# Optimization experiments

Measured on AMD Instinct MI355X. Metric: run time of the kernel, lower is better.

## Reference

```python
import jax, jax.numpy as jnp
import numpy as np


def gcn_conv(x, W, b, src, dst, num_nodes):
    # PyG GCNConv: h = D^{-1/2} (A + I) D^{-1/2} (x W) + b
    h = x @ W  # [N, H]
    ones = jnp.ones(src.shape[0], dtype=h.dtype)
    deg = jax.ops.segment_sum(ones, dst, num_segments=num_nodes) + 1.0  # +1 for self-loop
    d_inv_sqrt = jax.lax.rsqrt(deg)
    norm = d_inv_sqrt[src] * d_inv_sqrt[dst]  # [E]
    msg = h[src] * norm[:, None]  # [E, H] gather
    agg = jax.ops.segment_sum(msg, dst, num_segments=num_nodes)  # scatter-add
    agg = agg + h * (1.0 / deg)[:, None]  # self-loop term: deg_i^{-1/2} * deg_i^{-1/2}
    return agg + b


def setup_inputs() -> dict:
    key = jax.random.key(0)
    ks = jax.random.split(key, 10)
    N, E, F, H, C, G = 100000, 1000000, 64, 128, 2, 512
    x = jax.random.normal(ks[0], (N, F), dtype=jnp.float32)
    edge_index = jax.random.randint(ks[1], (2, E), 0, N, dtype=jnp.int64)
    batch = jnp.sort(jax.random.randint(ks[2], (N,), 0, G, dtype=jnp.int64))
    s1 = 1.0 / np.sqrt(F)
    s2 = 1.0 / np.sqrt(H)
    W1 = jax.random.normal(ks[3], (F, H), dtype=jnp.float32) * s1
    b1 = jnp.zeros((H,), dtype=jnp.float32)
    W2 = jax.random.normal(ks[4], (H, H), dtype=jnp.float32) * s2
    b2 = jnp.zeros((H,), dtype=jnp.float32)
    Wfc = jax.random.normal(ks[5], (H, C), dtype=jnp.float32) * s2
    bfc = jnp.zeros((C,), dtype=jnp.float32)
    return {"x": x, "edge_index": edge_index, "batch": batch, "num_graphs": G,
            "W1": W1, "b1": b1, "W2": W2, "b2": b2, "Wfc": Wfc, "bfc": bfc}


def reference(x, edge_index, batch, num_graphs, W1, b1, W2, b2, Wfc, bfc):
    # Dropout is inference-mode (identity), matching model.eval().
    N = x.shape[0]
    src, dst = edge_index[0], edge_index[1]
    h = gcn_conv(x, W1, b1, src, dst, N)
    h = jax.nn.relu(h)
    h = gcn_conv(h, W2, b2, src, dst, N)
    h = jax.nn.relu(h)
    # global mean pool over graphs
    summed = jax.ops.segment_sum(h, batch, num_segments=num_graphs)  # [G, H]
    counts = jax.ops.segment_sum(jnp.ones((N,), h.dtype), batch, num_segments=num_graphs)
    pooled = summed / jnp.maximum(counts, 1.0)[:, None]
    logits = pooled @ Wfc + bfc  # [G, C]
    return jax.nn.softmax(logits, axis=1)
```

## Files before the change

### kernel.cpp

```cpp
#include <hip/hip_runtime.h>
#include <hip/hip_bf16.h>

typedef __hip_bfloat16 bf16;
typedef __attribute__((ext_vector_type(8))) short short8;
typedef __attribute__((ext_vector_type(4))) float f32x4;
typedef __attribute__((ext_vector_type(2))) float f32x2;

#define FDIM 64
#define HDIM 128

#define ESTRIDE 4096
#define EC 8192
#define ECPT (EC / 256)

__device__ __forceinline__ float b2f(bf16 v) { return __bfloat162float(v); }
__device__ __forceinline__ float bits2f(unsigned int u) {
    return __uint_as_float(u << 16);
}
__device__ __forceinline__ unsigned short f2bits(float f) {
    bf16 b = __float2bfloat16(f);
    return *reinterpret_cast<unsigned short*>(&b);
}
__device__ __forceinline__ unsigned char f2fp8(float v) {
    int pk = __builtin_amdgcn_cvt_pk_fp8_f32(v, v, 0, false);
    return (unsigned char)(pk & 0xFF);
}

__global__ __launch_bounds__(256) void k_prep_flags(const unsigned short* __restrict__ w1u,
                                                    const int* __restrict__ edge,
                                                    const int* __restrict__ batch,
                                                    int* __restrict__ flags,
                                                    int* __restrict__ zbase, int zn4) {
    if (blockIdx.x == 0 && threadIdx.x < 192) {
        int wave = threadIdx.x >> 6, lane = threadIdx.x & 63;
        if (wave == 0) {
            int wild = 0;
#pragma unroll
            for (int r = 0; r < 2; r++) {
                int i = 2 * lane + 128 * r;
                int e = (w1u[i] >> 7) & 0xFF;
                wild += (e == 0 || e >= 137) ? 1 : 0;
            }
            for (int s = 32; s; s >>= 1) wild += __shfl_down(wild, s);
            if (lane == 0) flags[0] = (wild > 16) ? 1 : 0;
        } else if (wave == 1) {
            int z = 0;
#pragma unroll
            for (int r = 0; r < 2; r++) {
                int i = 2 * lane + 1 + 128 * r;
                z += (edge[i] == 0) ? 1 : 0;
            }
            for (int s = 32; s; s >>= 1) z += __shfl_down(z, s);
            if (lane == 0) flags[1] = (z > 64) ? 1 : 0;
        } else {
            int z = 0;
#pragma unroll
            for (int r = 0; r < 2; r++) {
                int i = 1025 + 2 * lane + 128 * r;
                z += (batch[i] == 0) ? 1 : 0;
            }
            for (int s = 32; s; s >>= 1) z += __shfl_down(z, s);
            if (lane == 0) flags[2] = (z > 64) ? 1 : 0;
        }
    }
    int4 zz = make_int4(0, 0, 0, 0);
    int stride = gridDim.x * 256;
    for (int t = blockIdx.x * 256 + threadIdx.x; t < zn4; t += stride)
        ((int4*)zbase)[t] = zz;
}

__device__ __forceinline__ int edge_word(const int* e, long long logical_idx, int is64) {
    return is64 ? e[2 * logical_idx] : e[logical_idx];
}

__global__ __launch_bounds__(256) void k_phase1(const int* __restrict__ edge,
                                                int* __restrict__ gcur,
                                                int* __restrict__ ebuf,
                                                int E,
                                                const void* __restrict__ W1, const void* __restrict__ b1,
                                                const void* __restrict__ W2, const void* __restrict__ b2,
                                                const void* __restrict__ Wfc, const void* __restrict__ bfc,
                                                bf16* __restrict__ W1t, bf16* __restrict__ W2t,
                                                bf16* __restrict__ b1c, bf16* __restrict__ b2c,
                                                bf16* __restrict__ Wfcc, bf16* __restrict__ bfcc,
                                                const void* __restrict__ x,
                                                unsigned char* __restrict__ X8,
                                                int totalX4, const int* __restrict__ flags,
                                                const int* __restrict__ batch,
                                                int* __restrict__ gstart,
                                                int N, int G,
                                                int NB1, int WB, int XB) {
    int blk = blockIdx.x;
    if (blk < NB1) {
        __shared__ int h[512];
        int tid = threadIdx.x;
        for (int b2 = tid; b2 < 512; b2 += 256) h[b2] = 0;
        __syncthreads();
        int is64 = flags[1];
        int e0 = blk * EC;
        int dcache[ECPT];
#pragma unroll
        for (int k = 0; k < ECPT; k++) {
            int i = e0 + (k << 8) + tid;
            int d = -1;
            if (i < E) d = edge_word(edge, (long long)E + i, is64);
            dcache[k] = d;
            if (d >= 0) atomicAdd(&h[(d >> 8) & 511], 1);
        }
        __syncthreads();
        for (int b2 = tid; b2 < 512; b2 += 256) {
            int c = h[b2];
            h[b2] = c ? atomicAdd(&gcur[b2], c) : 0;
        }
        __syncthreads();
#pragma unroll
        for (int k = 0; k < ECPT; k++) {
            int i = e0 + (k << 8) + tid;
            int d = dcache[k];
            if (d >= 0) {
                int s = edge_word(edge, i, is64);
                int bb = (d >> 8) & 511;
                int pos = atomicAdd(&h[bb], 1);
                if ((unsigned)pos < (unsigned)ESTRIDE)
                    ebuf[(bb << 12) + pos] = s | ((d & 255) << 24);
            }
        }
    } else if (blk < NB1 + WB) {
        int f0 = flags[0];
        int gid = (blk - NB1) * 256 + threadIdx.x;
        int stride = WB * 256;
#define CV(src, si) (f0 ? __float2bfloat16(((const float*)(src))[si]) : ((const bf16*)(src))[si])
        for (int i = gid; i < FDIM * HDIM; i += stride) {
            int n = i >> 6, k = i & 63;
            W1t[i] = CV(W1, k * HDIM + n);
        }
        for (int i = gid; i < HDIM * HDIM; i += stride) {
            int n = i >> 7, k = i & 127;
            W2t[i] = CV(W2, k * HDIM + n);
        }
        for (int i = gid; i < HDIM; i += stride) b1c[i] = CV(b1, i);
        for (int i = gid; i < HDIM; i += stride) b2c[i] = CV(b2, i);
        for (int i = gid; i < HDIM * 2; i += stride) Wfcc[i] = CV(Wfc, i);
        for (int i = gid; i < 2; i += stride) bfcc[i] = CV(bfc, i);
#undef CV
    } else if (blk < NB1 + WB + XB) {
        int t = (blk - NB1 - WB) * 256 + threadIdx.x;
        if (t >= totalX4) return;
        float4 v;
        if (flags[0]) {
            v = ((const float4*)x)[t];
        } else {
            uint2 p = ((const uint2*)x)[t];
            v.x = bits2f(p.x & 0xFFFFu); v.y = bits2f(p.x >> 16);
            v.z = bits2f(p.y & 0xFFFFu); v.w = bits2f(p.y >> 16);
        }
        unsigned int q0 = (unsigned int)__builtin_amdgcn_cvt_pk_fp8_f32(v.x, v.y, 0, false) & 0xFFFFu;
        unsigned int q1 = (unsigned int)__builtin_amdgcn_cvt_pk_fp8_f32(v.z, v.w, 0, false) & 0xFFFFu;
        ((unsigned int*)X8)[t] = (q1 << 16) | q0;
    } else {
        int i = (blk - NB1 - WB - XB) * 256 + threadIdx.x;
        if (i >= N) return;
        int is64 = flags[2];
        int bi = is64 ? batch[2 * i] : batch[i];
        if (i == 0) {
            for (int g = 0; g <= bi; g++) gstart[g] = 0;
        } else {
            int bp = is64 ? batch[2 * (i - 1)] : batch[i - 1];
            for (int g = bp + 1; g <= bi; g++) gstart[g] = i;
        }
        if (i == N - 1) {
            for (int g = bi + 1; g <= G; g++) gstart[g] = N;
        }
    }
}

__global__ __launch_bounds__(256) void k_csr(const int* __restrict__ ebuf,
                                             const int* __restrict__ gcur,
                                             int* __restrict__ rowptr,
                                             int* __restrict__ cnt,
                                             float* __restrict__ dinv,
                                             int* __restrict__ srclist,
                                             int N) {
    __shared__ int sred[256];
    __shared__ int sc[256];
    __shared__ int sa[256], sb[256];
    int b = blockIdx.x;
    int tid = threadIdx.x;
    int part = 0;
    for (int j = tid; j < b; j += 256) {
        int v = gcur[j];
        part += (v > ESTRIDE) ? ESTRIDE : v;
    }
    sred[tid] = part;
    __syncthreads();
    for (int s = 128; s > 0; s >>= 1) {
        if (tid < s) sred[tid] += sred[tid + s];
        __syncthreads();
    }
    int gbase = sred[0];
    int cnt_b = gcur[b];
    if (cnt_b > ESTRIDE) cnt_b = ESTRIDE;
    sc[tid] = 0;
    __syncthreads();
    const int* eb = ebuf + (b << 12);
    for (int j = tid; j < cnt_b; j += 256) {
        int p = eb[j];
        atomicAdd(&sc[(unsigned)p >> 24], 1);
    }
    __syncthreads();
    int cval = sc[tid];
    sa[tid] = cval;
    __syncthreads();
    int* cur = sa; int* nxt = sb;
    for (int off = 1; off < 256; off <<= 1) {
        int v = cur[tid];
        if (tid >= off) v += cur[tid - off];
        nxt[tid] = v;
        __syncthreads();
        int* t = cur; cur = nxt; nxt = t;
    }
    int excl = cur[tid] - cval;
    int node = (b << 8) + tid;
    if (node < N) {
        rowptr[node] = gbase + excl;
        cnt[node] = cval;
        dinv[node] = rsqrtf((float)cval + 1.0f);
    }
    __syncthreads();
    sc[tid] = excl;
    __syncthreads();
    for (int j = tid; j < cnt_b; j += 256) {
        int p = eb[j];
        int pos = atomicAdd(&sc[(unsigned)p >> 24], 1);
        srclist[gbase + pos] = p & 0xFFFFFF;
    }
}

#define ACCFP8(u2, e) do { \
    f32x2 f01 = __builtin_amdgcn_cvt_pk_f32_fp8((u2).x, false); \
    f32x2 f23 = __builtin_amdgcn_cvt_pk_f32_fp8((u2).x, true); \
    f32x2 f45 = __builtin_amdgcn_cvt_pk_f32_fp8((u2).y, false); \
    f32x2 f67 = __builtin_amdgcn_cvt_pk_f32_fp8((u2).y, true); \
    acc[0] += f01[0] * (e); acc[1] += f01[1] * (e); \
    acc[2] += f23[0] * (e); acc[3] += f23[1] * (e); \
    acc[4] += f45[0] * (e); acc[5] += f45[1] * (e); \
    acc[6] += f67[0] * (e); acc[7] += f67[1] * (e); } while (0)

#define K1PAD 72
__global__ __launch_bounds__(256) void k_agg_gemmA(const unsigned char* __restrict__ x8,
                                                   const int* __restrict__ srclist,
                                                   const int* __restrict__ rowptr,
                                                   const int* __restrict__ count,
                                                   const float* __restrict__ dinv,
                                                   const bf16* __restrict__ W1t,
                                                   const bf16* __restrict__ bias,
                                                   unsigned char* __restrict__ h8, int N) {
    __shared__ bf16 As[64 * K1PAD];
    __shared__ bf16 Wt[HDIM * K1PAD];
    __shared__ float bsf[HDIM];
    int tid = threadIdx.x;
    int base = blockIdx.x * 64;
    {
        const uint4* wsrc = (const uint4*)W1t;
        for (int i = tid; i < HDIM * 8; i += 256) {
            int n = i >> 3, c = i & 7;
            *(uint4*)&Wt[n * K1PAD + c * 8] = wsrc[n * 8 + c];
        }
    }
    if (tid < HDIM) bsf[tid] = b2f(bias[tid]);
    int wave = tid >> 6, lane = tid & 63;
    int group = lane >> 3, sub = lane & 7, lb = group << 3;
    const uint2* hrow = (const uint2*)x8;
#pragma unroll
    for (int pass = 0; pass < 2; pass++) {
        int r = pass * 32 + wave * 8 + group;
        int i = base + r;
        float acc[8] = {0.f, 0.f, 0.f, 0.f, 0.f, 0.f, 0.f, 0.f};
        if (i < N) {
            int start = rowptr[i];
            int cnt = count[i];
            float di = dinv[i];
            for (int jb = 0; jb < cnt; jb += 8) {
                int m = cnt - jb; if (m > 8) m = 8;
                int sv = srclist[start + jb + ((sub < m) ? sub : (m - 1))];
                float dvv = dinv[sv];
                if (m == 8) {
                    int s[8]; float e[8]; uint2 v[8];
#pragma unroll
                    for (int t = 0; t < 8; t++) { s[t] = __shfl(sv, lb + t); e[t] = __shfl(dvv, lb + t); }
#pragma unroll
                    for (int t = 0; t < 8; t++) v[t] = hrow[(size_t)s[t] * 8 + sub];
#pragma unroll
                    for (int t = 0; t < 8; t++) ACCFP8(v[t], e[t]);
                } else {
                    int j = 0;
                    for (; j + 4 <= m; j += 4) {
                        int s0 = __shfl(sv, lb + j + 0); float e0 = __shfl(dvv, lb + j + 0);
                        int s1 = __shfl(sv, lb + j + 1); float e1 = __shfl(dvv, lb + j + 1);
                        int s2 = __shfl(sv, lb + j + 2); float e2 = __shfl(dvv, lb + j + 2);
                        int s3 = __shfl(sv, lb + j + 3); float e3 = __shfl(dvv, lb + j + 3);
                        uint2 v0 = hrow[(size_t)s0 * 8 + sub];
                        uint2 v1 = hrow[(size_t)s1 * 8 + sub];
                        uint2 v2 = hrow[(size_t)s2 * 8 + sub];
                        uint2 v3 = hrow[(size_t)s3 * 8 + sub];
                        ACCFP8(v0, e0); ACCFP8(v1, e1); ACCFP8(v2, e2); ACCFP8(v3, e3);
                    }
                    for (; j < m; j++) {
                        int s0 = __shfl(sv, lb + j); float e0 = __shfl(dvv, lb + j);
                        uint2 v0 = hrow[(size_t)s0 * 8 + sub];
                        ACCFP8(v0, e0);
                    }
                }
            }
            uint2 vs = hrow[(size_t)i * 8 + sub];
            float self = di * di;
            float sacc[8] = {0.f};
            {
                float* acc = sacc;
                ACCFP8(vs, self);
            }
#pragma unroll
            for (int k = 0; k < 8; k++) acc[k] = di * acc[k] + sacc[k];
        }
        uint4 pv;
        pv.x = ((unsigned int)f2bits(acc[1]) << 16) | f2bits(acc[0]);
        pv.y = ((unsigned int)f2bits(acc[3]) << 16) | f2bits(acc[2]);
        pv.z = ((unsigned int)f2bits(acc[5]) << 16) | f2bits(acc[4]);
        pv.w = ((unsigned int)f2bits(acc[7]) << 16) | f2bits(acc[6]);
        *(uint4*)&As[r * K1PAD + sub * 8] = pv;
    }
    __syncthreads();
    int l15 = lane & 15, q = lane >> 4;
    int m0 = wave * 16;
    short8 af[2];
#pragma unroll
    for (int kc = 0; kc < 2; kc++)
        af[kc] = *(const short8*)&As[(m0 + l15) * K1PAD + kc * 32 + q * 8];
    f32x4 acc[8];
#pragma unroll
    for (int nt = 0; nt < 8; nt++) {
        acc[nt] = (f32x4){0.f, 0.f, 0.f, 0.f};
#pragma unroll
        for (int kc = 0; kc < 2; kc++) {
            short8 bf = *(const short8*)&Wt[(nt * 16 + l15) * K1PAD + kc * 32 + q * 8];
            acc[nt] = __builtin_amdgcn_mfma_f32_16x16x32_bf16(af[kc], bf, acc[nt], 0, 0, 0);
        }
    }
#pragma unroll
    for (int nt = 0; nt < 8; nt++) {
        int col = nt * 16 + l15;
        float bv = bsf[col];
#pragma unroll
        for (int r = 0; r < 4; r++) {
            int gr = base + m0 + q * 4 + r;
            if (gr < N) {
                float v = fmaxf(acc[nt][r] + bv, 0.f);
                h8[(size_t)gr * HDIM + col] = f2fp8(v);
            }
        }
    }
}

__global__ __launch_bounds__(256) void k_agg128(const unsigned char* __restrict__ h8,
                                                const int* __restrict__ srclist,
                                                const int* __restrict__ rowptr,
                                                const int* __restrict__ count,
                                                const float* __restrict__ dinv,
                                                bf16* __restrict__ outb, int N) {
    int wave = threadIdx.x >> 6;
    int lane = threadIdx.x & 63;
    int group = lane >> 4;
    int sub = lane & 15;
    int i = blockIdx.x * 16 + wave * 4 + group;
    if (i >= N) return;
    int start = rowptr[i];
    int cnt = count[i];
    float di = dinv[i];
    const uint2* hrow = (const uint2*)h8;
    float acc[8] = {0.f, 0.f, 0.f, 0.f, 0.f, 0.f, 0.f, 0.f};
    int lb = group << 4;
    for (int jb = 0; jb < cnt; jb += 16) {
        int m = cnt - jb; if (m > 16) m = 16;
        int sv = srclist[start + jb + ((sub < m) ? sub : (m - 1))];
        float dvv = dinv[sv];
        int j = 0;
        for (; j + 8 <= m; j += 8) {
            int s[8]; float e[8]; uint2 v[8];
#pragma unroll
            for (int t = 0; t < 8; t++) { s[t] = __shfl(sv, lb + j + t); e[t] = __shfl(dvv, lb + j + t); }
#pragma unroll
            for (int t = 0; t < 8; t++) v[t] = hrow[(size_t)s[t] * 16 + sub];
#pragma unroll
            for (int t = 0; t < 8; t++) ACCFP8(v[t], e[t]);
        }
        for (; j + 4 <= m; j += 4) {
            int s0 = __shfl(sv, lb + j + 0); float e0 = __shfl(dvv, lb + j + 0);
            int s1 = __shfl(sv, lb + j + 1); float e1 = __shfl(dvv, lb + j + 1);
            int s2 = __shfl(sv, lb + j + 2); float e2 = __shfl(dvv, lb + j + 2);
            int s3 = __shfl(sv, lb + j + 3); float e3 = __shfl(dvv, lb + j + 3);
            uint2 v0 = hrow[(size_t)s0 * 16 + sub];
            uint2 v1 = hrow[(size_t)s1 * 16 + sub];
            uint2 v2 = hrow[(size_t)s2 * 16 + sub];
            uint2 v3 = hrow[(size_t)s3 * 16 + sub];
            ACCFP8(v0, e0); ACCFP8(v1, e1); ACCFP8(v2, e2); ACCFP8(v3, e3);
        }
        for (; j < m; j++) {
            int s0 = __shfl(sv, lb + j); float e0 = __shfl(dvv, lb + j);
            uint2 v0 = hrow[(size_t)s0 * 16 + sub];
            ACCFP8(v0, e0);
        }
    }
    {
        uint2 vs = hrow[(size_t)i * 16 + sub];
        float self = di * di;
        float sacc[8] = {0.f};
        {
            float* acc = sacc;
            ACCFP8(vs, self);
        }
#pragma unroll
        for (int k = 0; k < 8; k++) acc[k] = di * acc[k] + sacc[k];
    }
    uint4 pv;
    pv.x = ((unsigned int)f2bits(acc[1]) << 16) | f2bits(acc[0]);
    pv.y = ((unsigned int)f2bits(acc[3]) << 16) | f2bits(acc[2]);
    pv.z = ((unsigned int)f2bits(acc[5]) << 16) | f2bits(acc[4]);
    pv.w = ((unsigned int)f2bits(acc[7]) << 16) | f2bits(acc[6]);
    ((uint4*)outb)[(size_t)i * 16 + sub] = pv;
}

#define K2PAD 136
__global__ __launch_bounds__(256) void k_gemmB(const bf16* __restrict__ Z,
                                               const bf16* __restrict__ W2t,
                                               const bf16* __restrict__ bias,
                                               bf16* __restrict__ outp, int N) {
    __shared__ bf16 As[64 * K2PAD];
    __shared__ bf16 Wt[HDIM * K2PAD];
    __shared__ float bsf[HDIM];
    int tid = threadIdx.x;
    int base = blockIdx.x * 64;
    {
        const uint4* wsrc = (const uint4*)W2t;
        for (int i = tid; i < HDIM * 16; i += 256) {
            int n = i >> 4, c = i & 15;
            *(uint4*)&Wt[n * K2PAD + c * 8] = wsrc[n * 16 + c];
        }
    }
    const uint4* xb = (const uint4*)Z;
    for (int i = tid; i < 64 * 16; i += 256) {
        int r = i >> 4, c = i & 15;
        int gr = base + r; if (gr >= N) gr = N - 1;
        *(uint4*)&As[r * K2PAD + c * 8] = xb[(size_t)gr * 16 + c];
    }
    if (tid < HDIM) bsf[tid] = b2f(bias[tid]);
    __syncthreads();
    int wid = tid >> 6, lane = tid & 63;
    int l15 = lane & 15, q = lane >> 4;
    int m0 = wid * 16;
    short8 af[4];
#pragma unroll
    for (int kc = 0; kc < 4; kc++)
        af[kc] = *(const short8*)&As[(m0 + l15) * K2PAD + kc * 32 + q * 8];
    f32x4 acc[8];
#pragma unroll
    for (int nt = 0; nt < 8; nt++) {
        acc[nt] = (f32x4){0.f, 0.f, 0.f, 0.f};
#pragma unroll
        for (int kc = 0; kc < 4; kc++) {
            short8 bf = *(const short8*)&Wt[(nt * 16 + l15) * K2PAD + kc * 32 + q * 8];
            acc[nt] = __builtin_amdgcn_mfma_f32_16x16x32_bf16(af[kc], bf, acc[nt], 0, 0, 0);
        }
    }
#pragma unroll
    for (int nt = 0; nt < 8; nt++) {
        int col = nt * 16 + l15;
        float bv = bsf[col];
#pragma unroll
        for (int r = 0; r < 4; r++) {
            int gr = base + m0 + q * 4 + r;
            if (gr < N) outp[(size_t)gr * HDIM + col] = __float2bfloat16(fmaxf(acc[nt][r] + bv, 0.f));
        }
    }
}

__global__ __launch_bounds__(256) void k_pool(const bf16* __restrict__ hact,
                                              const int* __restrict__ gstart,
                                              const bf16* __restrict__ Wfc,
                                              const bf16* __restrict__ bfc,
                                              void* __restrict__ out,
                                              const int* __restrict__ flags) {
    __shared__ float lds[16][HDIM + 1];
    __shared__ float colsum[HDIM];
    int g = blockIdx.x;
    int s = gstart[g], e = gstart[g + 1];
    int tid = threadIdx.x;
    int cslot = tid & 15;
    int rslot = tid >> 4;
    const uint4* hp = (const uint4*)hact;
    float a[8] = {0.f, 0.f, 0.f, 0.f, 0.f, 0.f, 0.f, 0.f};
    for (int r = s + rslot; r < e; r += 16) {
        uint4 v = hp[(size_t)r * 16 + cslot];
        a[0] += bits2f(v.x & 0xFFFFu); a[1] += bits2f(v.x >> 16);
        a[2] += bits2f(v.y & 0xFFFFu); a[3] += bits2f(v.y >> 16);
        a[4] += bits2f(v.z & 0xFFFFu); a[5] += bits2f(v.z >> 16);
        a[6] += bits2f(v.w & 0xFFFFu); a[7] += bits2f(v.w >> 16);
    }
#pragma unroll
    for (int k = 0; k < 8; k++) lds[rslot][cslot * 8 + k] = a[k];
    __syncthreads();
    if (tid < HDIM) {
        float sum = 0.f;
#pragma unroll
        for (int k = 0; k < 16; k++) sum += lds[k][tid];
        colsum[tid] = sum;
    }
    __syncthreads();
    if (tid >= 64) return;
    int lane = tid;
    float inv = 1.0f / fmaxf((float)(e - s), 1.0f);
    float m0 = colsum[2 * lane] * inv;
    float m1 = colsum[2 * lane + 1] * inv;
    float l0 = m0 * b2f(Wfc[(2 * lane) * 2 + 0]) + m1 * b2f(Wfc[(2 * lane + 1) * 2 + 0]);
    float l1 = m0 * b2f(Wfc[(2 * lane) * 2 + 1]) + m1 * b2f(Wfc[(2 * lane + 1) * 2 + 1]);
    for (int sft = 32; sft; sft >>= 1) { l0 += __shfl_down(l0, sft); l1 += __shfl_down(l1, sft); }
    if (lane == 0) {
        float z0 = l0 + b2f(bfc[0]);
        float z1 = l1 + b2f(bfc[1]);
        float mx = fmaxf(z0, z1);
        float e0 = expf(z0 - mx), e1 = expf(z1 - mx);
        float sm = e0 + e1;
        float p0 = e0 / sm, p1 = e1 / sm;
        if (flags[0]) {
            ((float*)out)[2 * g + 0] = p0;
            ((float*)out)[2 * g + 1] = p1;
        } else {
            ((bf16*)out)[2 * g + 0] = __float2bfloat16(p0);
            ((bf16*)out)[2 * g + 1] = __float2bfloat16(p1);
        }
    }
}

extern "C" void kernel_launch(void* const* d_in, const int* in_sizes, int n_in,
                              void* d_out, int out_size, void* d_ws, size_t ws_size,
                              hipStream_t stream) {
    const void* x    = d_in[0];
    const int*  edge = (const int*)d_in[1];
    const int*  batch= (const int*)d_in[2];
    const void* W1  = d_in[4];
    const void* b1  = d_in[5];
    const void* W2  = d_in[6];
    const void* b2  = d_in[7];
    const void* Wfc = d_in[8];
    const void* bfc = d_in[9];

    int N = in_sizes[0] / FDIM;
    int E = in_sizes[1] / 2;
    int G = out_size / 2;

    int*   flags  = (int*)d_ws;
    float* dinv   = (float*)((char*)d_ws + 64);
    int*   gcur   = (int*)(dinv + N);
    int*   gstart = gcur + 512;
    int*   rowptr = gstart + 516;
    int*   count  = rowptr + N;
    int*   srclist= count + N;
    int*   ebuf   = srclist + E;
    bf16*  Zbuf   = (bf16*)(ebuf + 512 * ESTRIDE);
    bf16*  Bbuf   = Zbuf + (size_t)N * HDIM;
    bf16*  b1c    = Bbuf + (size_t)N * HDIM;
    bf16*  b2c    = b1c + HDIM;
    bf16*  Wfcc   = b2c + HDIM;
    bf16*  bfcc   = Wfcc + 256;
    bf16*  W1t    = bfcc + 64;
    bf16*  W2t    = W1t + FDIM * HDIM;
    unsigned char* H8 = (unsigned char*)(W2t + HDIM * HDIM);
    unsigned char* X8 = H8 + (size_t)N * HDIM;

    int NB  = (N + 255) >> 8;
    int NB1 = (E + EC - 1) / EC;
    int WB = 32;
    int XB = (N * 16 + 255) / 256;
    int BB = (N + 255) / 256;
    int totalX4 = N * 16;
    int zn4 = 512 / 4;

    k_prep_flags<<<4, 256, 0, stream>>>((const unsigned short*)W1, edge, batch, flags,
                                        gcur, zn4);
    k_phase1<<<NB1 + WB + XB + BB, 256, 0, stream>>>(edge, gcur, ebuf, E,
                                                     W1, b1, W2, b2, Wfc, bfc,
                                                     W1t, W2t, b1c, b2c, Wfcc, bfcc,
                                                     x, X8, totalX4, flags,
                                                     batch, gstart, N, G,
                                                     NB1, WB, XB);
    k_csr<<<NB, 256, 0, stream>>>(ebuf, gcur, rowptr, count, dinv, srclist, N);

    k_agg_gemmA<<<(N + 63) / 64, 256, 0, stream>>>(X8, srclist, rowptr, count, dinv,
                                                   W1t, b1c, H8, N);
    k_agg128<<<(N + 15) / 16, 256, 0, stream>>>(H8, srclist, rowptr, count, dinv, Zbuf, N);
    k_gemmB<<<(N + 63) / 64, 256, 0, stream>>>(Zbuf, W2t, b2c, Bbuf, N);

    k_pool<<<G, 256, 0, stream>>>(Bbuf, gstart, Wfcc, bfcc, d_out, flags);
}
```

Baseline: 238.4 us.

## Degree-sort nodes per block and split fused layer-1 aggregation from its GEMM

k_csr now builds a per-256-node permutation that orders nodes by descending in-degree (capped at 32). Both aggregation kernels walk nodes in that order so the groups sharing a wave have similar edge counts, which reduces divergence and load imbalance. The fused layer-1 aggregate+GEMM kernel is split into a standalone gather kernel (k_agg64) and a separate MFMA GEMM kernel. The split adds a bf16 intermediate write and read plus one extra launch. The flag-detection kernel is removed: each block in phase1 now infers input dtypes itself with a ballot, and a memset replaces the old zeroing.

```diff
diff --git a/kernel.cpp b/kernel.cpp
--- a/kernel.cpp
+++ b/kernel.cpp
@@ -24,49 +24,6 @@
 __device__ __forceinline__ unsigned char f2fp8(float v) {
     int pk = __builtin_amdgcn_cvt_pk_fp8_f32(v, v, 0, false);
     return (unsigned char)(pk & 0xFF);
-}
-
-__global__ __launch_bounds__(256) void k_prep_flags(const unsigned short* __restrict__ w1u,
-                                                    const int* __restrict__ edge,
-                                                    const int* __restrict__ batch,
-                                                    int* __restrict__ flags,
-                                                    int* __restrict__ zbase, int zn4) {
-    if (blockIdx.x == 0 && threadIdx.x < 192) {
-        int wave = threadIdx.x >> 6, lane = threadIdx.x & 63;
-        if (wave == 0) {
-            int wild = 0;
-#pragma unroll
-            for (int r = 0; r < 2; r++) {
-                int i = 2 * lane + 128 * r;
-                int e = (w1u[i] >> 7) & 0xFF;
-                wild += (e == 0 || e >= 137) ? 1 : 0;
-            }
-            for (int s = 32; s; s >>= 1) wild += __shfl_down(wild, s);
-            if (lane == 0) flags[0] = (wild > 16) ? 1 : 0;
-        } else if (wave == 1) {
-            int z = 0;
-#pragma unroll
-            for (int r = 0; r < 2; r++) {
-                int i = 2 * lane + 1 + 128 * r;
-                z += (edge[i] == 0) ? 1 : 0;
-            }
-            for (int s = 32; s; s >>= 1) z += __shfl_down(z, s);
-            if (lane == 0) flags[1] = (z > 64) ? 1 : 0;
-        } else {
-            int z = 0;
-#pragma unroll
-            for (int r = 0; r < 2; r++) {
-                int i = 1025 + 2 * lane + 128 * r;
-                z += (batch[i] == 0) ? 1 : 0;
-            }
-            for (int s = 32; s; s >>= 1) z += __shfl_down(z, s);
-            if (lane == 0) flags[2] = (z > 64) ? 1 : 0;
-        }
-    }
-    int4 zz = make_int4(0, 0, 0, 0);
-    int stride = gridDim.x * 256;
-    for (int t = blockIdx.x * 256 + threadIdx.x; t < zn4; t += stride)
-        ((int4*)zbase)[t] = zz;
 }
 
 __device__ __forceinline__ int edge_word(const int* e, long long logical_idx, int is64) {
@@ -85,18 +42,20 @@
                                                 bf16* __restrict__ Wfcc, bf16* __restrict__ bfcc,
                                                 const void* __restrict__ x,
                                                 unsigned char* __restrict__ X8,
-                                                int totalX4, const int* __restrict__ flags,
+                                                int totalX4,
+                                                int* __restrict__ flags,
                                                 const int* __restrict__ batch,
                                                 int* __restrict__ gstart,
                                                 int N, int G,
                                                 int NB1, int WB, int XB) {
     int blk = blockIdx.x;
+    int tid = threadIdx.x;
     if (blk < NB1) {
+        unsigned long long zb = __ballot(edge[2 * (tid & 63) + 1] == 0);
+        int is64 = (__popcll(zb) > 32);
         __shared__ int h[512];
-        int tid = threadIdx.x;
         for (int b2 = tid; b2 < 512; b2 += 256) h[b2] = 0;
         __syncthreads();
-        int is64 = flags[1];
         int e0 = blk * EC;
         int dcache[ECPT];
 #pragma unroll
@@ -126,8 +85,13 @@
             }
         }
     } else if (blk < NB1 + WB) {
-        int f0 = flags[0];
-        int gid = (blk - NB1) * 256 + threadIdx.x;
+        const unsigned short* w1u = (const unsigned short*)W1;
+        unsigned short wv = w1u[2 * (tid & 63)];
+        int ee = (wv >> 7) & 0xFF;
+        unsigned long long wb2 = __ballot(ee == 0 || ee >= 137);
+        int f0 = (__popcll(wb2) > 4);
+        if (blk == NB1 && tid == 0) flags[0] = f0;
+        int gid = (blk - NB1) * 256 + tid;
         int stride = WB * 256;
 #define CV(src, si) (f0 ? __float2bfloat16(((const float*)(src))[si]) : ((const bf16*)(src))[si])
         for (int i = gid; i < FDIM * HDIM; i += stride) {
@@ -144,10 +108,15 @@
         for (int i = gid; i < 2; i += stride) bfcc[i] = CV(bfc, i);
 #undef CV
     } else if (blk < NB1 + WB + XB) {
-        int t = (blk - NB1 - WB) * 256 + threadIdx.x;
+        const unsigned short* w1u = (const unsigned short*)W1;
+        unsigned short wv = w1u[2 * (tid & 63)];
+        int ee = (wv >> 7) & 0xFF;
+        unsigned long long wb2 = __ballot(ee == 0 || ee >= 137);
+        int f0 = (__popcll(wb2) > 4);
+        int t = (blk - NB1 - WB) * 256 + tid;
         if (t >= totalX4) return;
         float4 v;
-        if (flags[0]) {
+        if (f0) {
             v = ((const float4*)x)[t];
         } else {
             uint2 p = ((const uint2*)x)[t];
@@ -158,9 +127,11 @@
         unsigned int q1 = (unsigned int)__builtin_amdgcn_cvt_pk_fp8_f32(v.z, v.w, 0, false) & 0xFFFFu;
         ((unsigned int*)X8)[t] = (q1 << 16) | q0;
     } else {
-        int i = (blk - NB1 - WB - XB) * 256 + threadIdx.x;
+        int bv = batch[1025 + 2 * (tid & 63)];
+        unsigned long long bb2 = __ballot(bv == 0);
+        int is64 = (__popcll(bb2) > 32);
+        int i = (blk - NB1 - WB - XB) * 256 + tid;
         if (i >= N) return;
-        int is64 = flags[2];
         int bi = is64 ? batch[2 * i] : batch[i];
         if (i == 0) {
             for (int g = 0; g <= bi; g++) gstart[g] = 0;
@@ -180,10 +151,12 @@
                                              int* __restrict__ cnt,
                                              float* __restrict__ dinv,
                                              int* __restrict__ srclist,
+                                             int* __restrict__ perm,
                                              int N) {
     __shared__ int sred[256];
     __shared__ int sc[256];
     __shared__ int sa[256], sb[256];
+    __shared__ int dh[33];
     int b = blockIdx.x;
     int tid = threadIdx.x;
     int part = 0;
@@ -233,6 +206,25 @@
         int p = eb[j];
         int pos = atomicAdd(&sc[(unsigned)p >> 24], 1);
         srclist[gbase + pos] = p & 0xFFFFFF;
+    }
+    if (tid < 33) dh[tid] = 0;
+    perm[(b << 8) + tid] = N;
+    __syncthreads();
+    int bin = -1;
+    if (node < N) {
+        int c = (cval < 32) ? cval : 32;
+        bin = 32 - c;
+        atomicAdd(&dh[bin], 1);
+    }
+    __syncthreads();
+    if (tid == 0) {
+        int acc2 = 0;
+        for (int k = 0; k < 33; k++) { int t = dh[k]; dh[k] = acc2; acc2 += t; }
+    }
+    __syncthreads();
+    if (bin >= 0) {
+        int pos = atomicAdd(&dh[bin], 1);
+        perm[(b << 8) + pos] = node;
     }
 }
 
@@ -246,119 +238,75 @@
     acc[4] += f45[0] * (e); acc[5] += f45[1] * (e); \
     acc[6] += f67[0] * (e); acc[7] += f67[1] * (e); } while (0)
 
-#define K1PAD 72
-__global__ __launch_bounds__(256) void k_agg_gemmA(const unsigned char* __restrict__ x8,
-                                                   const int* __restrict__ srclist,
-                                                   const int* __restrict__ rowptr,
-                                                   const int* __restrict__ count,
-                                                   const float* __restrict__ dinv,
-                                                   const bf16* __restrict__ W1t,
-                                                   const bf16* __restrict__ bias,
-                                                   unsigned char* __restrict__ h8, int N) {
-    __shared__ bf16 As[64 * K1PAD];
-    __shared__ bf16 Wt[HDIM * K1PAD];
-    __shared__ float bsf[HDIM];
-    int tid = threadIdx.x;
-    int base = blockIdx.x * 64;
+__global__ __launch_bounds__(256) void k_agg64(const unsigned char* __restrict__ x8,
+                                               const int* __restrict__ srclist,
+                                               const int* __restrict__ rowptr,
+                                               const int* __restrict__ count,
+                                               const float* __restrict__ dinv,
+                                               const int* __restrict__ perm,
+                                               bf16* __restrict__ outb, int N, int NR) {
+    int wave = threadIdx.x >> 6;
+    int lane = threadIdx.x & 63;
+    int group = lane >> 3;
+    int sub = lane & 7;
+    int r = blockIdx.x * 32 + wave * 8 + group;
+    int i = (r < NR) ? perm[r] : N;
+    if (i >= N) return;
+    int start = rowptr[i];
+    int cnt = count[i];
+    float di = dinv[i];
+    const uint2* hrow = (const uint2*)x8;
+    float acc[8] = {0.f, 0.f, 0.f, 0.f, 0.f, 0.f, 0.f, 0.f};
+    int lb = group << 3;
+    for (int jb = 0; jb < cnt; jb += 8) {
+        int m = cnt - jb; if (m > 8) m = 8;
+        int sv = srclist[start + jb + ((sub < m) ? sub : (m - 1))];
+        float dvv = dinv[sv];
+        if (m == 8) {
+            int s[8]; float e[8]; uint2 v[8];
+#pragma unroll
+            for (int t = 0; t < 8; t++) { s[t] = __shfl(sv, lb + t); e[t] = __shfl(dvv, lb + t); }
+#pragma unroll
+            for (int t = 0; t < 8; t++) v[t] = hrow[(size_t)s[t] * 8 + sub];
+#pragma unroll
+            for (int t = 0; t < 8; t++) ACCFP8(v[t], e[t]);
+        } else {
+            int j = 0;
+            for (; j + 4 <= m; j += 4) {
+                int s0 = __shfl(sv, lb + j + 0); float e0 = __shfl(dvv, lb + j + 0);
+                int s1 = __shfl(sv, lb + j + 1); float e1 = __shfl(dvv, lb + j + 1);
+                int s2 = __shfl(sv, lb + j + 2); float e2 = __shfl(dvv, lb + j + 2);
+                int s3 = __shfl(sv, lb + j + 3); float e3 = __shfl(dvv, lb + j + 3);
+                uint2 v0 = hrow[(size_t)s0 * 8 + sub];
+                uint2 v1 = hrow[(size_t)s1 * 8 + sub];
+                uint2 v2 = hrow[(size_t)s2 * 8 + sub];
+                uint2 v3 = hrow[(size_t)s3 * 8 + sub];
+                ACCFP8(v0, e0); ACCFP8(v1, e1); ACCFP8(v2, e2); ACCFP8(v3, e3);
+            }
+            for (; j < m; j++) {
+                int s0 = __shfl(sv, lb + j); float e0 = __shfl(dvv, lb + j);
+                uint2 v0 = hrow[(size_t)s0 * 8 + sub];
+                ACCFP8(v0, e0);
+            }
+        }
+    }
     {
-        const uint4* wsrc = (const uint4*)W1t;
-        for (int i = tid; i < HDIM * 8; i += 256) {
-            int n = i >> 3, c = i & 7;
-            *(uint4*)&Wt[n * K1PAD + c * 8] = wsrc[n * 8 + c];
-        }
-    }
-    if (tid < HDIM) bsf[tid] = b2f(bias[tid]);
-    int wave = tid >> 6, lane = tid & 63;
-    int group = lane >> 3, sub = lane & 7, lb = group << 3;
-    const uint2* hrow = (const uint2*)x8;
-#pragma unroll
-    for (int pass = 0; pass < 2; pass++) {
-        int r = pass * 32 + wave * 8 + group;
-        int i = base + r;
-        float acc[8] = {0.f, 0.f, 0.f, 0.f, 0.f, 0.f, 0.f, 0.f};
-        if (i < N) {
-            int start = rowptr[i];
-            int cnt = count[i];
-            float di = dinv[i];
-            for (int jb = 0; jb < cnt; jb += 8) {
-                int m = cnt - jb; if (m > 8) m = 8;
-                int sv = srclist[start + jb + ((sub < m) ? sub : (m - 1))];
-                float dvv = dinv[sv];
-                if (m == 8) {
-                    int s[8]; float e[8]; uint2 v[8];
-#pragma unroll
-                    for (int t = 0; t < 8; t++) { s[t] = __shfl(sv, lb + t); e[t] = __shfl(dvv, lb + t); }
-#pragma unroll
-                    for (int t = 0; t < 8; t++) v[t] = hrow[(size_t)s[t] * 8 + sub];
-#pragma unroll
-                    for (int t = 0; t < 8; t++) ACCFP8(v[t], e[t]);
-                } else {
-                    int j = 0;
-                    for (; j + 4 <= m; j += 4) {
-                        int s0 = __shfl(sv, lb + j + 0); float e0 = __shfl(dvv, lb + j + 0);
-                        int s1 = __shfl(sv, lb + j + 1); float e1 = __shfl(dvv, lb + j + 1);
-                        int s2 = __shfl(sv, lb + j + 2); float e2 = __shfl(dvv, lb + j + 2);
-                        int s3 = __shfl(sv, lb + j + 3); float e3 = __shfl(dvv, lb + j + 3);
-                        uint2 v0 = hrow[(size_t)s0 * 8 + sub];
-                        uint2 v1 = hrow[(size_t)s1 * 8 + sub];
-                        uint2 v2 = hrow[(size_t)s2 * 8 + sub];
-                        uint2 v3 = hrow[(size_t)s3 * 8 + sub];
-                        ACCFP8(v0, e0); ACCFP8(v1, e1); ACCFP8(v2, e2); ACCFP8(v3, e3);
-                    }
-                    for (; j < m; j++) {
-                        int s0 = __shfl(sv, lb + j); float e0 = __shfl(dvv, lb + j);
-                        uint2 v0 = hrow[(size_t)s0 * 8 + sub];
-                        ACCFP8(v0, e0);
-                    }
-                }
-            }
-            uint2 vs = hrow[(size_t)i * 8 + sub];
-            float self = di * di;
-            float sacc[8] = {0.f};
-            {
-                float* acc = sacc;
-                ACCFP8(vs, self);
-            }
-#pragma unroll
-            for (int k = 0; k < 8; k++) acc[k] = di * acc[k] + sacc[k];
-        }
-        uint4 pv;
-        pv.x = ((unsigned int)f2bits(acc[1]) << 16) | f2bits(acc[0]);
-        pv.y = ((unsigned int)f2bits(acc[3]) << 16) | f2bits(acc[2]);
-        pv.z = ((unsigned int)f2bits(acc[5]) << 16) | f2bits(acc[4]);
-        pv.w = ((unsigned int)f2bits(acc[7]) << 16) | f2bits(acc[6]);
-        *(uint4*)&As[r * K1PAD + sub * 8] = pv;
-    }
-    __syncthreads();
-    int l15 = lane & 15, q = lane >> 4;
-    int m0 = wave * 16;
-    short8 af[2];
-#pragma unroll
-    for (int kc = 0; kc < 2; kc++)
-        af[kc] = *(const short8*)&As[(m0 + l15) * K1PAD + kc * 32 + q * 8];
-    f32x4 acc[8];
-#pragma unroll
-    for (int nt = 0; nt < 8; nt++) {
-        acc[nt] = (f32x4){0.f, 0.f, 0.f, 0.f};
-#pragma unroll
-        for (int kc = 0; kc < 2; kc++) {
-            short8 bf = *(const short8*)&Wt[(nt * 16 + l15) * K1PAD + kc * 32 + q * 8];
-            acc[nt] = __builtin_amdgcn_mfma_f32_16x16x32_bf16(af[kc], bf, acc[nt], 0, 0, 0);
-        }
-    }
-#pragma unroll
-    for (int nt = 0; nt < 8; nt++) {
-        int col = nt * 16 + l15;
-        float bv = bsf[col];
-#pragma unroll
-        for (int r = 0; r < 4; r++) {
-            int gr = base + m0 + q * 4 + r;
-            if (gr < N) {
-                float v = fmaxf(acc[nt][r] + bv, 0.f);
-                h8[(size_t)gr * HDIM + col] = f2fp8(v);
-            }
-        }
-    }
+        uint2 vs = hrow[(size_t)i * 8 + sub];
+        float self = di * di;
+        float sacc[8] = {0.f};
+        {
+            float* acc = sacc;
+            ACCFP8(vs, self);
+        }
+#pragma unroll
+        for (int k = 0; k < 8; k++) acc[k] = di * acc[k] + sacc[k];
+    }
+    uint4 pv;
+    pv.x = ((unsigned int)f2bits(acc[1]) << 16) | f2bits(acc[0]);
+    pv.y = ((unsigned int)f2bits(acc[3]) << 16) | f2bits(acc[2]);
+    pv.z = ((unsigned int)f2bits(acc[5]) << 16) | f2bits(acc[4]);
+    pv.w = ((unsigned int)f2bits(acc[7]) << 16) | f2bits(acc[6]);
+    ((uint4*)outb)[(size_t)i * 8 + sub] = pv;
 }
 
 __global__ __launch_bounds__(256) void k_agg128(const unsigned char* __restrict__ h8,
@@ -366,12 +314,14 @@
                                                 const int* __restrict__ rowptr,
                                                 const int* __restrict__ count,
                                                 const float* __restrict__ dinv,
-                                                bf16* __restrict__ outb, int N) {
+                                                const int* __restrict__ perm,
+                                                bf16* __restrict__ outb, int N, int NR) {
     int wave = threadIdx.x >> 6;
     int lane = threadIdx.x & 63;
     int group = lane >> 4;
     int sub = lane & 15;
-    int i = blockIdx.x * 16 + wave * 4 + group;
+    int r = blockIdx.x * 16 + wave * 4 + group;
+    int i = (r < NR) ? perm[r] : N;
     if (i >= N) return;
     int start = rowptr[i];
     int cnt = count[i];
@@ -427,6 +377,65 @@
     pv.z = ((unsigned int)f2bits(acc[5]) << 16) | f2bits(acc[4]);
     pv.w = ((unsigned int)f2bits(acc[7]) << 16) | f2bits(acc[6]);
     ((uint4*)outb)[(size_t)i * 16 + sub] = pv;
+}
+
+#define K1PAD 72
+__global__ __launch_bounds__(256) void k_gemmA(const bf16* __restrict__ Y,
+                                               const bf16* __restrict__ W1t,
+                                               const bf16* __restrict__ bias,
+                                               unsigned char* __restrict__ h8, int N) {
+    __shared__ bf16 As[64 * K1PAD];
+    __shared__ bf16 Wt[HDIM * K1PAD];
+    __shared__ float bsf[HDIM];
+    int tid = threadIdx.x;
+    int base = blockIdx.x * 64;
+    {
+        const uint4* wsrc = (const uint4*)W1t;
+        for (int i = tid; i < HDIM * 8; i += 256) {
+            int n = i >> 3, c = i & 7;
+            *(uint4*)&Wt[n * K1PAD + c * 8] = wsrc[n * 8 + c];
+        }
+    }
+    {
+        const uint4* xb = (const uint4*)Y;
+        for (int i = tid; i < 64 * 8; i += 256) {
+            int r = i >> 3, c = i & 7;
+            int gr = base + r; if (gr >= N) gr = N - 1;
+            *(uint4*)&As[r * K1PAD + c * 8] = xb[(size_t)gr * 8 + c];
+        }
+    }
+    if (tid < HDIM) bsf[tid] = b2f(bias[tid]);
+    __syncthreads();
+    int wid = tid >> 6, lane = tid & 63;
+    int l15 = lane & 15, q = lane >> 4;
+    int m0 = wid * 16;
+    short8 af[2];
+#pragma unroll
+    for (int kc = 0; kc < 2; kc++)
+        af[kc] = *(const short8*)&As[(m0 + l15) * K1PAD + kc * 32 + q * 8];
+    f32x4 acc[8];
+#pragma unroll
+    for (int nt = 0; nt < 8; nt++) {
+        acc[nt] = (f32x4){0.f, 0.f, 0.f, 0.f};
+#pragma unroll
+        for (int kc = 0; kc < 2; kc++) {
+            short8 bf = *(const short8*)&Wt[(nt * 16 + l15) * K1PAD + kc * 32 + q * 8];
+            acc[nt] = __builtin_amdgcn_mfma_f32_16x16x32_bf16(af[kc], bf, acc[nt], 0, 0, 0);
+        }
+    }
+#pragma unroll
+    for (int nt = 0; nt < 8; nt++) {
+        int col = nt * 16 + l15;
+        float bv = bsf[col];
+#pragma unroll
+        for (int r = 0; r < 4; r++) {
+            int gr = base + m0 + q * 4 + r;
+            if (gr < N) {
+                float v = fmaxf(acc[nt][r] + bv, 0.f);
+                h8[(size_t)gr * HDIM + col] = f2fp8(v);
+            }
+        }
+    }
 }
 
 #define K2PAD 136
@@ -563,10 +572,11 @@
     int*   gstart = gcur + 512;
     int*   rowptr = gstart + 516;
     int*   count  = rowptr + N;
-    int*   srclist= count + N;
+    int*   perm_  = count + N;
+    int*   srclist= perm_ + 131072;
     int*   ebuf   = srclist + E;
-    bf16*  Zbuf   = (bf16*)(ebuf + 512 * ESTRIDE);
-    bf16*  Bbuf   = Zbuf + (size_t)N * HDIM;
+    bf16*  Abuf   = (bf16*)(ebuf + 512 * ESTRIDE);
+    bf16*  Bbuf   = Abuf + (size_t)N * HDIM;
     bf16*  b1c    = Bbuf + (size_t)N * HDIM;
     bf16*  b2c    = b1c + HDIM;
     bf16*  Wfcc   = b2c + HDIM;
@@ -576,28 +586,31 @@
     unsigned char* H8 = (unsigned char*)(W2t + HDIM * HDIM);
     unsigned char* X8 = H8 + (size_t)N * HDIM;
 
+    bf16* Y = Abuf;
+    bf16* Z = Abuf;
+
     int NB  = (N + 255) >> 8;
+    int NR  = NB << 8;
     int NB1 = (E + EC - 1) / EC;
     int WB = 32;
     int XB = (N * 16 + 255) / 256;
     int BB = (N + 255) / 256;
     int totalX4 = N * 16;
-    int zn4 = 512 / 4;
-
-    k_prep_flags<<<4, 256, 0, stream>>>((const unsigned short*)W1, edge, batch, flags,
-                                        gcur, zn4);
+
+    hipMemsetAsync(gcur, 0, 512 * sizeof(int), stream);
     k_phase1<<<NB1 + WB + XB + BB, 256, 0, stream>>>(edge, gcur, ebuf, E,
                                                      W1, b1, W2, b2, Wfc, bfc,
                                                      W1t, W2t, b1c, b2c, Wfcc, bfcc,
                                                      x, X8, totalX4, flags,
                                                      batch, gstart, N, G,
                                                      NB1, WB, XB);
-    k_csr<<<NB, 256, 0, stream>>>(ebuf, gcur, rowptr, count, dinv, srclist, N);
-
-    k_agg_gemmA<<<(N + 63) / 64, 256, 0, stream>>>(X8, srclist, rowptr, count, dinv,
-                                                   W1t, b1c, H8, N);
-    k_agg128<<<(N + 15) / 16, 256, 0, stream>>>(H8, srclist, rowptr, count, dinv, Zbuf, N);
-    k_gemmB<<<(N + 63) / 64, 256, 0, stream>>>(Zbuf, W2t, b2c, Bbuf, N);
+    k_csr<<<NB, 256, 0, stream>>>(ebuf, gcur, rowptr, count, dinv, srclist, perm_, N);
+
+    k_agg64<<<(NR + 31) / 32, 256, 0, stream>>>(X8, srclist, rowptr, count, dinv, perm_, Y, N, NR);
+    k_gemmA<<<(N + 63) / 64, 256, 0, stream>>>(Y, W1t, b1c, H8, N);
+
+    k_agg128<<<(NR + 15) / 16, 256, 0, stream>>>(H8, srclist, rowptr, count, dinv, perm_, Z, N, NR);
+    k_gemmB<<<(N + 63) / 64, 256, 0, stream>>>(Z, W2t, b2c, Bbuf, N);
 
     k_pool<<<G, 256, 0, stream>>>(Bbuf, gstart, Wfcc, bfcc, d_out, flags);
 }
```

Result: slower. 245.6 us (+3.0%).
